# Optimization experiments

Measured on AMD Instinct MI355X. Metric: run time of the kernel, lower is better.

## Reference

```python
import jax, jax.numpy as jnp
import numpy as np

D_INNER = 4096
DT_RANK = 128
D_STATE = 16
SEQ_LEN = 4096


def setup_inputs() -> dict:
    key = jax.random.key(0)
    kx, kin, kdel = jax.random.split(key, 3)
    x = jax.random.normal(kx, (SEQ_LEN, D_INNER), dtype=jnp.float32)
    # eqx.nn.Linear weights are [out_features, in_features]
    lim_in = 1.0 / np.sqrt(D_INNER)
    W_in = jax.random.uniform(kin, (DT_RANK + 2 * D_STATE, D_INNER),
                              minval=-lim_in, maxval=lim_in, dtype=jnp.float32)
    lim_d = 1.0 / np.sqrt(DT_RANK)
    W_delta = jax.random.uniform(kdel, (D_INNER, DT_RANK),
                                 minval=-lim_d, maxval=lim_d, dtype=jnp.float32)
    # A_log init exactly as in the module (deterministic)
    A = jnp.repeat(jnp.arange(1, D_STATE + 1), D_INNER).reshape(D_INNER, D_STATE)
    A_log = jnp.log(A.astype(jnp.float32))
    D = jnp.ones((D_INNER,), dtype=jnp.float32)
    return {"x": x, "W_in": W_in, "W_delta": W_delta, "A_log": A_log, "D": D}


def selective_scan(x, delta, A, B, C, D):
    # x, delta: [L, d_inner]; A: [d_inner, d_state]; B, C: [L, d_state]; D: [d_inner]
    d_inner, d_state = A.shape
    delta_A = jnp.exp(jnp.einsum('ld,dn->ldn', delta, A))          # [L, d_inner, d_state]
    delta_B_u = jnp.einsum('ld,ln,ld->ldn', delta, B, x)           # [L, d_inner, d_state]

    def step(h, inp):
        dA, dBu, c = inp
        h = dA * h + dBu                                           # [d_inner, d_state]
        y = jnp.einsum('dn,n->d', h, c)
        return h, y

    h0 = jnp.zeros((d_inner, d_state), dtype=x.dtype)
    _, ys = jax.lax.scan(step, h0, (delta_A, delta_B_u, C))
    return ys + x * D


def reference(x, W_in, W_delta, A_log, D):
    A = -jnp.exp(A_log)
    dbc = x @ W_in.T                                               # [L, dt_rank + 2*d_state]
    delta, B, C = jnp.split(dbc, [DT_RANK, DT_RANK + D_STATE], axis=-1)
    delta = jax.nn.softplus(delta @ W_delta.T)                     # [L, d_inner]
    return selective_scan(x, delta, A, B, C, D)
```

## Files before the change

kernel.cpp:

```cpp
#include <hip/hip_runtime.h>
#include <math.h>
#include <stdint.h>

#define L_SEQ   4096
#define DI      4096
#define RNK     128
#define NS      16
#define NCOL    160
#define GCH     32
#define CLEN    128
#define KSPLIT  16

#define DBC_SLICE 655360
#define PART_OFF  655360
#define BF_OFF    4849664
#define DSZ       524288

typedef __attribute__((ext_vector_type(8))) short bf16x8;
typedef __attribute__((ext_vector_type(4))) float f32x4;

__device__ __forceinline__ float fast_exp2(float v) {
#if __has_builtin(__builtin_amdgcn_exp2f)
  return __builtin_amdgcn_exp2f(v);
#else
  return exp2f(v);
#endif
}

__device__ __forceinline__ unsigned short f2bf(float f) {
  uint32_t u = __float_as_uint(f);
  uint32_t r = (u + 0x7FFFu + ((u >> 16) & 1u)) >> 16;
  return (unsigned short)r;
}
__device__ __forceinline__ float bf2f(unsigned short b) {
  return __uint_as_float(((uint32_t)b) << 16);
}

__global__ __launch_bounds__(256) void gemm1_kernel(const float* __restrict__ x,
                                                    const float* __restrict__ Win,
                                                    float* __restrict__ parts) {
  __shared__ float xs[64][36];
  __shared__ float wsh[160][36];
  const int t  = threadIdx.x;
  const int tx = t & 15, ty = t >> 4;
  const int mt = blockIdx.x >> 4;
  const int ks = blockIdx.x & 15;
  const int row0 = mt * 64;
  const int kbase0 = ks * 256;

  float acc[4][10];
#pragma unroll
  for (int r = 0; r < 4; ++r)
#pragma unroll
    for (int c = 0; c < 10; ++c) acc[r][c] = 0.f;

  for (int kc = 0; kc < 8; ++kc) {
    const int kb = kbase0 + kc * 32;
#pragma unroll
    for (int i = 0; i < 2; ++i) {
      int f = t + i * 256;
      int r = f >> 3, c4 = (f & 7) * 4;
      *(float4*)&xs[r][c4] = *(const float4*)&x[(row0 + r) * 4096 + kb + c4];
    }
#pragma unroll
    for (int i = 0; i < 5; ++i) {
      int f = t + i * 256;
      int r = f >> 3, c4 = (f & 7) * 4;
      *(float4*)&wsh[r][c4] = *(const float4*)&Win[r * 4096 + kb + c4];
    }
    __syncthreads();
#pragma unroll
    for (int kk = 0; kk < 8; ++kk) {
      float4 xv[4];
#pragma unroll
      for (int r = 0; r < 4; ++r) xv[r] = *(float4*)&xs[ty * 4 + r][kk * 4];
#pragma unroll
      for (int c = 0; c < 10; ++c) {
        float4 wv = *(float4*)&wsh[tx + 16 * c][kk * 4];
#pragma unroll
        for (int r = 0; r < 4; ++r) {
          acc[r][c] = fmaf(xv[r].x, wv.x, acc[r][c]);
          acc[r][c] = fmaf(xv[r].y, wv.y, acc[r][c]);
          acc[r][c] = fmaf(xv[r].z, wv.z, acc[r][c]);
          acc[r][c] = fmaf(xv[r].w, wv.w, acc[r][c]);
        }
      }
    }
    __syncthreads();
  }
  float* outp = parts + ks * DBC_SLICE;
#pragma unroll
  for (int r = 0; r < 4; ++r)
#pragma unroll
    for (int c = 0; c < 10; ++c)
      outp[(row0 + ty * 4 + r) * NCOL + tx + 16 * c] = acc[r][c];
}

__global__ __launch_bounds__(256) void reduce_dbc_kernel(const float* __restrict__ parts,
                                                         float* __restrict__ dbc,
                                                         unsigned short* __restrict__ dbch,
                                                         unsigned short* __restrict__ dbcl) {
  const int i = (blockIdx.x * 256 + threadIdx.x) * 4;
  float4 a = *(const float4*)&parts[i];
#pragma unroll
  for (int s = 1; s < KSPLIT; ++s) {
    float4 b = *(const float4*)&parts[(size_t)s * DBC_SLICE + i];
    a.x += b.x; a.y += b.y; a.z += b.z; a.w += b.w;
  }
  const int row = i / NCOL;
  const int col = i - row * NCOL;
  if (col < RNK) {
    float v[4] = {a.x, a.y, a.z, a.w};
    ushort4 h, lo;
    unsigned short* hp = (unsigned short*)&h;
    unsigned short* lp = (unsigned short*)&lo;
#pragma unroll
    for (int q = 0; q < 4; ++q) {
      hp[q] = f2bf(v[q]);
      lp[q] = f2bf(v[q] - bf2f(hp[q]));
    }
    *(ushort4*)&dbch[row * RNK + col] = h;
    *(ushort4*)&dbcl[row * RNK + col] = lo;
  } else {
    *(float4*)&dbc[i] = a;
  }
}

__global__ __launch_bounds__(256) void split_wd_kernel(const float* __restrict__ Wd,
                                                       unsigned short* __restrict__ Wdh,
                                                       unsigned short* __restrict__ Wdl) {
  const int i = (blockIdx.x * 256 + threadIdx.x) * 4;
  float4 a = *(const float4*)&Wd[i];
  float v[4] = {a.x, a.y, a.z, a.w};
  ushort4 h, lo;
  unsigned short* hp = (unsigned short*)&h;
  unsigned short* lp = (unsigned short*)&lo;
#pragma unroll
  for (int q = 0; q < 4; ++q) {
    hp[q] = f2bf(v[q]);
    lp[q] = f2bf(v[q] - bf2f(hp[q]));
  }
  *(ushort4*)&Wdh[i] = h;
  *(ushort4*)&Wdl[i] = lo;
}

__global__ __launch_bounds__(256) void gemm2_kernel(const unsigned short* __restrict__ dbch,
                                                    const unsigned short* __restrict__ dbcl,
                                                    const unsigned short* __restrict__ Wdh,
                                                    const unsigned short* __restrict__ Wdl,
                                                    float* __restrict__ delta_out) {
  const int t  = threadIdx.x;
  const int w  = t >> 6, l = t & 63;
  const int lr = l & 15;
  const int lk = l >> 4;
  const int mt = blockIdx.x & 63, nt = blockIdx.x >> 6;
  const int wr = w >> 1, wc = w & 1;
  const int m0 = mt * 64 + wr * 32;
  const int n0 = nt * 128 + wc * 64;

  f32x4 acc[2][4];
#pragma unroll
  for (int i = 0; i < 2; ++i)
#pragma unroll
    for (int j = 0; j < 4; ++j)
      acc[i][j] = (f32x4){0.f, 0.f, 0.f, 0.f};

#pragma unroll
  for (int ks = 0; ks < 4; ++ks) {
    const int k0 = ks * 32 + lk * 8;
    bf16x8 ah[2], al_[2], bh[4], bl[4];
#pragma unroll
    for (int i = 0; i < 2; ++i) {
      ah[i]  = *(const bf16x8*)&dbch[(m0 + i * 16 + lr) * RNK + k0];
      al_[i] = *(const bf16x8*)&dbcl[(m0 + i * 16 + lr) * RNK + k0];
    }
#pragma unroll
    for (int j = 0; j < 4; ++j) {
      bh[j] = *(const bf16x8*)&Wdh[(n0 + j * 16 + lr) * RNK + k0];
      bl[j] = *(const bf16x8*)&Wdl[(n0 + j * 16 + lr) * RNK + k0];
    }
#pragma unroll
    for (int i = 0; i < 2; ++i)
#pragma unroll
      for (int j = 0; j < 4; ++j) {
        acc[i][j] = __builtin_amdgcn_mfma_f32_16x16x32_bf16(ah[i],  bh[j], acc[i][j], 0, 0, 0);
        acc[i][j] = __builtin_amdgcn_mfma_f32_16x16x32_bf16(ah[i],  bl[j], acc[i][j], 0, 0, 0);
        acc[i][j] = __builtin_amdgcn_mfma_f32_16x16x32_bf16(al_[i], bh[j], acc[i][j], 0, 0, 0);
      }
  }

#pragma unroll
  for (int i = 0; i < 2; ++i)
#pragma unroll
    for (int j = 0; j < 4; ++j)
#pragma unroll
      for (int r = 0; r < 4; ++r) {
        const int row = m0 + i * 16 + lk * 4 + r;
        const int col = n0 + j * 16 + lr;
        float v = acc[i][j][r];
        float sp = (v > 20.f) ? v : log1pf(__expf(v));
        delta_out[row * 4096 + col] = sp;
      }
}

__global__ __launch_bounds__(256) void scan1_kernel(const float* __restrict__ delta,
                                                    const float* __restrict__ x,
                                                    const float* __restrict__ A_log,
                                                    const float* __restrict__ dbc,
                                                    float* __restrict__ part) {
  __shared__ float Bs[CLEN][NS];
  const int t = threadIdx.x;
  const int d = blockIdx.x * 256 + t;
  const int g = blockIdx.y;
  const int l0 = g * CLEN;
#pragma unroll
  for (int i = 0; i < 8; ++i) {
    int f = t + i * 256;
    int l = f >> 4, n = f & 15;
    Bs[l][n] = dbc[(l0 + l) * NCOL + RNK + n];
  }
  __syncthreads();

  float al2[NS];
#pragma unroll
  for (int n = 0; n < NS; ++n) al2[n] = -expf(A_log[d * NS + n]) * 1.44269504f;
  bool uni = true;
#pragma unroll
  for (int n = 1; n < NS; ++n) uni = uni && (al2[n] == al2[0]);

  float h[NS], P[NS];
#pragma unroll
  for (int n = 0; n < NS; ++n) { h[n] = 0.f; P[n] = 1.f; }

  if (uni) {
    const float a0 = al2[0];
    float Ps = 1.f;
    for (int l = 0; l < CLEN; ++l) {
      float dv = delta[(l0 + l) * 4096 + d];
      float xv = x[(l0 + l) * 4096 + d];
      float dx = dv * xv;
      float dA = fast_exp2(dv * a0);
      Ps *= dA;
      const float4* br = (const float4*)Bs[l];
      float4 b0 = br[0], b1 = br[1], b2 = br[2], b3 = br[3];
      h[0]  = fmaf(dA, h[0],  dx * b0.x); h[1]  = fmaf(dA, h[1],  dx * b0.y);
      h[2]  = fmaf(dA, h[2],  dx * b0.z); h[3]  = fmaf(dA, h[3],  dx * b0.w);
      h[4]  = fmaf(dA, h[4],  dx * b1.x); h[5]  = fmaf(dA, h[5],  dx * b1.y);
      h[6]  = fmaf(dA, h[6],  dx * b1.z); h[7]  = fmaf(dA, h[7],  dx * b1.w);
      h[8]  = fmaf(dA, h[8],  dx * b2.x); h[9]  = fmaf(dA, h[9],  dx * b2.y);
      h[10] = fmaf(dA, h[10], dx * b2.z); h[11] = fmaf(dA, h[11], dx * b2.w);
      h[12] = fmaf(dA, h[12], dx * b3.x); h[13] = fmaf(dA, h[13], dx * b3.y);
      h[14] = fmaf(dA, h[14], dx * b3.z); h[15] = fmaf(dA, h[15], dx * b3.w);
    }
#pragma unroll
    for (int n = 0; n < NS; ++n) P[n] = Ps;
  } else {
    for (int l = 0; l < CLEN; ++l) {
      float dv = delta[(l0 + l) * 4096 + d];
      float xv = x[(l0 + l) * 4096 + d];
      float dx = dv * xv;
#pragma unroll
      for (int n = 0; n < NS; ++n) {
        float dA = fast_exp2(dv * al2[n]);
        h[n] = fmaf(dA, h[n], dx * Bs[l][n]);
        P[n] *= dA;
      }
    }
  }
  float* pg = part + (size_t)g * 32 * 4096;
#pragma unroll
  for (int n = 0; n < NS; ++n) {
    pg[n * 4096 + d] = P[n];
    pg[(NS + n) * 4096 + d] = h[n];
  }
}

__global__ __launch_bounds__(256) void scan2_kernel(float* __restrict__ part) {
  const int idx = blockIdx.x * 256 + threadIdx.x;
  const int d = idx & 4095;
  const int n = idx >> 12;
  float h = 0.f;
  for (int g = 0; g < GCH; ++g) {
    float* pg = part + (size_t)g * 32 * 4096;
    float Pv = pg[n * 4096 + d];
    float Hv = pg[(NS + n) * 4096 + d];
    float nh = fmaf(Pv, h, Hv);
    pg[n * 4096 + d] = h;
    h = nh;
  }
}

__global__ __launch_bounds__(256) void scan3_kernel(float* io,
                                                    const float* __restrict__ x,
                                                    const float* __restrict__ A_log,
                                                    const float* __restrict__ dbc,
                                                    const float* __restrict__ Dvec,
                                                    const float* __restrict__ part) {
  __shared__ float Bs[CLEN][NS];
  __shared__ float Cs[CLEN][NS];
  const int t = threadIdx.x;
  const int d = blockIdx.x * 256 + t;
  const int g = blockIdx.y;
  const int l0 = g * CLEN;
#pragma unroll
  for (int i = 0; i < 8; ++i) {
    int f = t + i * 256;
    int l = f >> 4, n = f & 15;
    Bs[l][n] = dbc[(l0 + l) * NCOL + RNK + n];
    Cs[l][n] = dbc[(l0 + l) * NCOL + RNK + NS + n];
  }
  __syncthreads();

  float al2[NS];
#pragma unroll
  for (int n = 0; n < NS; ++n) al2[n] = -expf(A_log[d * NS + n]) * 1.44269504f;
  bool uni = true;
#pragma unroll
  for (int n = 1; n < NS; ++n) uni = uni && (al2[n] == al2[0]);

  float h[NS];
  const float* pg = part + (size_t)g * 32 * 4096;
#pragma unroll
  for (int n = 0; n < NS; ++n) h[n] = pg[n * 4096 + d];
  const float Dd = Dvec[d];

  if (uni) {
    const float a0 = al2[0];
    for (int l = 0; l < CLEN; ++l) {
      float dv = io[(size_t)(l0 + l) * 4096 + d];
      float xv = x[(l0 + l) * 4096 + d];
      float dx = dv * xv;
      float dA = fast_exp2(dv * a0);
      const float4* br = (const float4*)Bs[l];
      const float4* cr = (const float4*)Cs[l];
      float4 b0 = br[0], b1 = br[1], b2 = br[2], b3 = br[3];
      float4 c0 = cr[0], c1 = cr[1], c2 = cr[2], c3 = cr[3];
      float y = 0.f;
      h[0]  = fmaf(dA, h[0],  dx * b0.x); y = fmaf(h[0],  c0.x, y);
      h[1]  = fmaf(dA, h[1],  dx * b0.y); y = fmaf(h[1],  c0.y, y);
      h[2]  = fmaf(dA, h[2],  dx * b0.z); y = fmaf(h[2],  c0.z, y);
      h[3]  = fmaf(dA, h[3],  dx * b0.w); y = fmaf(h[3],  c0.w, y);
      h[4]  = fmaf(dA, h[4],  dx * b1.x); y = fmaf(h[4],  c1.x, y);
      h[5]  = fmaf(dA, h[5],  dx * b1.y); y = fmaf(h[5],  c1.y, y);
      h[6]  = fmaf(dA, h[6],  dx * b1.z); y = fmaf(h[6],  c1.z, y);
      h[7]  = fmaf(dA, h[7],  dx * b1.w); y = fmaf(h[7],  c1.w, y);
      h[8]  = fmaf(dA, h[8],  dx * b2.x); y = fmaf(h[8],  c2.x, y);
      h[9]  = fmaf(dA, h[9],  dx * b2.y); y = fmaf(h[9],  c2.y, y);
      h[10] = fmaf(dA, h[10], dx * b2.z); y = fmaf(h[10], c2.z, y);
      h[11] = fmaf(dA, h[11], dx * b2.w); y = fmaf(h[11], c2.w, y);
      h[12] = fmaf(dA, h[12], dx * b3.x); y = fmaf(h[12], c3.x, y);
      h[13] = fmaf(dA, h[13], dx * b3.y); y = fmaf(h[13], c3.y, y);
      h[14] = fmaf(dA, h[14], dx * b3.z); y = fmaf(h[14], c3.z, y);
      h[15] = fmaf(dA, h[15], dx * b3.w); y = fmaf(h[15], c3.w, y);
      io[(size_t)(l0 + l) * 4096 + d] = fmaf(xv, Dd, y);
    }
  } else {
    for (int l = 0; l < CLEN; ++l) {
      float dv = io[(size_t)(l0 + l) * 4096 + d];
      float xv = x[(l0 + l) * 4096 + d];
      float dx = dv * xv;
      float y = 0.f;
#pragma unroll
      for (int n = 0; n < NS; ++n) {
        float dA = fast_exp2(dv * al2[n]);
        h[n] = fmaf(dA, h[n], dx * Bs[l][n]);
        y = fmaf(h[n], Cs[l][n], y);
      }
      io[(size_t)(l0 + l) * 4096 + d] = fmaf(xv, Dd, y);
    }
  }
}

extern "C" void kernel_launch(void* const* d_in, const int* in_sizes, int n_in,
                              void* d_out, int out_size, void* d_ws, size_t ws_size,
                              hipStream_t stream) {
  const float* x    = (const float*)d_in[0];
  const float* Win  = (const float*)d_in[1];
  const float* Wd   = (const float*)d_in[2];
  const float* Alog = (const float*)d_in[3];
  const float* Dv   = (const float*)d_in[4];
  float* out = (float*)d_out;
  float* ws  = (float*)d_ws;
  float* dbc  = ws;
  float* part = ws + PART_OFF;
  unsigned short* dbch = (unsigned short*)(ws + BF_OFF);
  unsigned short* dbcl = dbch + DSZ;
  unsigned short* wdh  = dbcl + DSZ;
  unsigned short* wdl  = wdh + DSZ;

  gemm1_kernel<<<1024, 256, 0, stream>>>(x, Win, out);
  reduce_dbc_kernel<<<640, 256, 0, stream>>>(out, dbc, dbch, dbcl);
  split_wd_kernel<<<512, 256, 0, stream>>>(Wd, wdh, wdl);
  gemm2_kernel<<<2048, 256, 0, stream>>>(dbch, dbcl, wdh, wdl, out);
  scan1_kernel<<<dim3(16, 32), 256, 0, stream>>>(out, x, Alog, dbc, part);
  scan2_kernel<<<256, 256, 0, stream>>>(part);
  scan3_kernel<<<dim3(16, 32), 256, 0, stream>>>(out, x, Alog, dbc, Dv, part);
}
```

Measured before the change: 375.4 us.

## Move first projection GEMM to bf16x3 MFMA with pre-split W_in

Replaces the fp32 LDS-tiled FMA GEMM for x @ W_in.T with MFMA 16x16x32 bf16 instructions, using a hi/lo bf16 split (three products) to keep near-fp32 accuracy. W_in is split into hi/lo bf16 arrays by a generalized split kernel that is also reused for W_delta. x is split on the fly in registers and both operands are loaded directly from global memory without shared memory. The goal is to cut the compute time of this GEMM, at the cost of an extra pre-pass over W_in and uncoalesced, unshared global loads.

```diff
diff --git a/kernel.cpp b/kernel.cpp
--- a/kernel.cpp
+++ b/kernel.cpp
@@ -14,7 +14,9 @@
 #define DBC_SLICE 655360
 #define PART_OFF  655360
 #define BF_OFF    4849664
+#define WIN_OFF   5898240
 #define DSZ       524288
+#define WSZ       655360
 
 typedef __attribute__((ext_vector_type(8))) short bf16x8;
 typedef __attribute__((ext_vector_type(4))) float f32x4;
@@ -36,64 +38,72 @@
   return __uint_as_float(((uint32_t)b) << 16);
 }
 
+__global__ __launch_bounds__(256) void split_pair_kernel(const float* __restrict__ src,
+                                                         unsigned short* __restrict__ dh,
+                                                         unsigned short* __restrict__ dl) {
+  const int i = (blockIdx.x * 256 + threadIdx.x) * 4;
+  float4 a = *(const float4*)&src[i];
+  float v[4] = {a.x, a.y, a.z, a.w};
+  ushort4 h, lo;
+  unsigned short* hp = (unsigned short*)&h;
+  unsigned short* lp = (unsigned short*)&lo;
+#pragma unroll
+  for (int q = 0; q < 4; ++q) {
+    hp[q] = f2bf(v[q]);
+    lp[q] = f2bf(v[q] - bf2f(hp[q]));
+  }
+  *(ushort4*)&dh[i] = h;
+  *(ushort4*)&dl[i] = lo;
+}
+
 __global__ __launch_bounds__(256) void gemm1_kernel(const float* __restrict__ x,
-                                                    const float* __restrict__ Win,
+                                                    const unsigned short* __restrict__ winh,
+                                                    const unsigned short* __restrict__ winl,
                                                     float* __restrict__ parts) {
-  __shared__ float xs[64][36];
-  __shared__ float wsh[160][36];
   const int t  = threadIdx.x;
-  const int tx = t & 15, ty = t >> 4;
+  const int w  = t >> 6, l = t & 63;
+  const int lr = l & 15;
+  const int lk = l >> 4;
   const int mt = blockIdx.x >> 4;
   const int ks = blockIdx.x & 15;
-  const int row0 = mt * 64;
-  const int kbase0 = ks * 256;
-
-  float acc[4][10];
-#pragma unroll
-  for (int r = 0; r < 4; ++r)
-#pragma unroll
-    for (int c = 0; c < 10; ++c) acc[r][c] = 0.f;
-
+  const int row = mt * 64 + w * 16 + lr;
+  const int kb  = ks * 256;
+
+  f32x4 acc[10];
+#pragma unroll
+  for (int j = 0; j < 10; ++j) acc[j] = (f32x4){0.f, 0.f, 0.f, 0.f};
+
+#pragma unroll
   for (int kc = 0; kc < 8; ++kc) {
-    const int kb = kbase0 + kc * 32;
-#pragma unroll
-    for (int i = 0; i < 2; ++i) {
-      int f = t + i * 256;
-      int r = f >> 3, c4 = (f & 7) * 4;
-      *(float4*)&xs[r][c4] = *(const float4*)&x[(row0 + r) * 4096 + kb + c4];
-    }
-#pragma unroll
-    for (int i = 0; i < 5; ++i) {
-      int f = t + i * 256;
-      int r = f >> 3, c4 = (f & 7) * 4;
-      *(float4*)&wsh[r][c4] = *(const float4*)&Win[r * 4096 + kb + c4];
-    }
-    __syncthreads();
-#pragma unroll
-    for (int kk = 0; kk < 8; ++kk) {
-      float4 xv[4];
-#pragma unroll
-      for (int r = 0; r < 4; ++r) xv[r] = *(float4*)&xs[ty * 4 + r][kk * 4];
-#pragma unroll
-      for (int c = 0; c < 10; ++c) {
-        float4 wv = *(float4*)&wsh[tx + 16 * c][kk * 4];
-#pragma unroll
-        for (int r = 0; r < 4; ++r) {
-          acc[r][c] = fmaf(xv[r].x, wv.x, acc[r][c]);
-          acc[r][c] = fmaf(xv[r].y, wv.y, acc[r][c]);
-          acc[r][c] = fmaf(xv[r].z, wv.z, acc[r][c]);
-          acc[r][c] = fmaf(xv[r].w, wv.w, acc[r][c]);
-        }
-      }
-    }
-    __syncthreads();
-  }
+    const int k0 = kb + kc * 32 + lk * 8;
+    float4 xa0 = *(const float4*)&x[row * 4096 + k0];
+    float4 xa1 = *(const float4*)&x[row * 4096 + k0 + 4];
+    float va[8] = {xa0.x, xa0.y, xa0.z, xa0.w, xa1.x, xa1.y, xa1.z, xa1.w};
+    bf16x8 ah, al_;
+#pragma unroll
+    for (int q = 0; q < 8; ++q) {
+      unsigned short hq = f2bf(va[q]);
+      ah[q]  = (short)hq;
+      al_[q] = (short)f2bf(va[q] - bf2f(hq));
+    }
+#pragma unroll
+    for (int j = 0; j < 10; ++j) {
+      const int col = j * 16 + lr;
+      bf16x8 bh = *(const bf16x8*)&winh[col * 4096 + k0];
+      bf16x8 bl = *(const bf16x8*)&winl[col * 4096 + k0];
+      acc[j] = __builtin_amdgcn_mfma_f32_16x16x32_bf16(ah,  bh, acc[j], 0, 0, 0);
+      acc[j] = __builtin_amdgcn_mfma_f32_16x16x32_bf16(ah,  bl, acc[j], 0, 0, 0);
+      acc[j] = __builtin_amdgcn_mfma_f32_16x16x32_bf16(al_, bh, acc[j], 0, 0, 0);
+    }
+  }
+
   float* outp = parts + ks * DBC_SLICE;
-#pragma unroll
-  for (int r = 0; r < 4; ++r)
-#pragma unroll
-    for (int c = 0; c < 10; ++c)
-      outp[(row0 + ty * 4 + r) * NCOL + tx + 16 * c] = acc[r][c];
+  const int r0 = mt * 64 + w * 16 + lk * 4;
+#pragma unroll
+  for (int j = 0; j < 10; ++j)
+#pragma unroll
+    for (int r = 0; r < 4; ++r)
+      outp[(r0 + r) * NCOL + j * 16 + lr] = acc[j][r];
 }
 
 __global__ __launch_bounds__(256) void reduce_dbc_kernel(const float* __restrict__ parts,
@@ -124,24 +134,6 @@
   } else {
     *(float4*)&dbc[i] = a;
   }
-}
-
-__global__ __launch_bounds__(256) void split_wd_kernel(const float* __restrict__ Wd,
-                                                       unsigned short* __restrict__ Wdh,
-                                                       unsigned short* __restrict__ Wdl) {
-  const int i = (blockIdx.x * 256 + threadIdx.x) * 4;
-  float4 a = *(const float4*)&Wd[i];
-  float v[4] = {a.x, a.y, a.z, a.w};
-  ushort4 h, lo;
-  unsigned short* hp = (unsigned short*)&h;
-  unsigned short* lp = (unsigned short*)&lo;
-#pragma unroll
-  for (int q = 0; q < 4; ++q) {
-    hp[q] = f2bf(v[q]);
-    lp[q] = f2bf(v[q] - bf2f(hp[q]));
-  }
-  *(ushort4*)&Wdh[i] = h;
-  *(ushort4*)&Wdl[i] = lo;
 }
 
 __global__ __launch_bounds__(256) void gemm2_kernel(const unsigned short* __restrict__ dbch,
@@ -387,10 +379,13 @@
   unsigned short* dbcl = dbch + DSZ;
   unsigned short* wdh  = dbcl + DSZ;
   unsigned short* wdl  = wdh + DSZ;
-
-  gemm1_kernel<<<1024, 256, 0, stream>>>(x, Win, out);
+  unsigned short* winh = (unsigned short*)(ws + WIN_OFF);
+  unsigned short* winl = winh + WSZ;
+
+  split_pair_kernel<<<640, 256, 0, stream>>>(Win, winh, winl);
+  split_pair_kernel<<<512, 256, 0, stream>>>(Wd, wdh, wdl);
+  gemm1_kernel<<<1024, 256, 0, stream>>>(x, winh, winl, out);
   reduce_dbc_kernel<<<640, 256, 0, stream>>>(out, dbc, dbch, dbcl);
-  split_wd_kernel<<<512, 256, 0, stream>>>(Wd, wdh, wdl);
   gemm2_kernel<<<2048, 256, 0, stream>>>(dbch, dbcl, wdh, wdl, out);
   scan1_kernel<<<dim3(16, 32), 256, 0, stream>>>(out, x, Alog, dbc, part);
   scan2_kernel<<<256, 256, 0, stream>>>(part);
```

Result: no change. 373.8 us (-0.4%).
